# Performance work log

Hardware: AMD Instinct MI355X
Metric: run time of the kernel (lower is better)

Reference implementation:

```python
import jax, jax.numpy as jnp
import numpy as np

HEADS = 8
HEAD_DIM = 64
INNER = HEADS * HEAD_DIM  # 512
DIM = 512
B, H, W = 8, 32, 32
KV_LEN, KV_DIM = 77, 1024


def group_norm(x, g, b, groups=32, eps=1e-6):
    # x: [B, C, H, W]
    Bx, C, Hx, Wx = x.shape
    xr = x.reshape(Bx, groups, C // groups, Hx, Wx)
    mu = xr.mean(axis=(2, 3, 4), keepdims=True)
    var = xr.var(axis=(2, 3, 4), keepdims=True)
    xr = (xr - mu) * jax.lax.rsqrt(var + eps)
    return xr.reshape(Bx, C, Hx, Wx) * g[None, :, None, None] + b[None, :, None, None]


def layer_norm(x, g, b, eps=1e-5):
    mu = x.mean(axis=-1, keepdims=True)
    var = x.var(axis=-1, keepdims=True)
    return (x - mu) * jax.lax.rsqrt(var + eps) * g + b


def attention(qx, kvx, Wq, Wk, Wv, Wo, bo):
    # qx: [B, Sq, dim_q], kvx: [B, Sk, dim_kv]
    q = qx @ Wq
    k = kvx @ Wk
    v = kvx @ Wv
    Bx, Sq, _ = q.shape
    Sk = k.shape[1]
    q = q.reshape(Bx, Sq, HEADS, HEAD_DIM)
    k = k.reshape(Bx, Sk, HEADS, HEAD_DIM)
    v = v.reshape(Bx, Sk, HEADS, HEAD_DIM)
    att = jnp.einsum('bqhd,bkhd->bhqk', q, k) * (HEAD_DIM ** -0.5)
    att = jax.nn.softmax(att.astype(jnp.float32), axis=-1).astype(q.dtype)
    o = jnp.einsum('bhqk,bkhd->bqhd', att, v).reshape(Bx, Sq, INNER)
    return o @ Wo + bo


def setup_inputs() -> dict:
    key = jax.random.key(0)
    ks = jax.random.split(key, 20)
    s = 0.02
    def n(k, shape):
        return jax.random.normal(k, shape, jnp.float32) * s
    return {
        'q': jax.random.normal(ks[0], (B, DIM, H, W), jnp.float32),
        'kv': jax.random.normal(ks[1], (B, KV_LEN, KV_DIM), jnp.float32),
        'gn_g': jnp.ones((DIM,), jnp.float32), 'gn_b': jnp.zeros((DIM,), jnp.float32),
        'ln2_g': jnp.ones((INNER,), jnp.float32), 'ln2_b': jnp.zeros((INNER,), jnp.float32),
        'ln3_g': jnp.ones((INNER,), jnp.float32), 'ln3_b': jnp.zeros((INNER,), jnp.float32),
        'ln4_g': jnp.ones((INNER,), jnp.float32), 'ln4_b': jnp.zeros((INNER,), jnp.float32),
        'fc_in_w': n(ks[2], (DIM, INNER)), 'fc_in_b': jnp.zeros((INNER,), jnp.float32),
        'fc_out_w': n(ks[3], (INNER, DIM)), 'fc_out_b': jnp.zeros((DIM,), jnp.float32),
        'a1_q': n(ks[4], (INNER, INNER)), 'a1_k': n(ks[5], (INNER, INNER)),
        'a1_v': n(ks[6], (INNER, INNER)), 'a1_o': n(ks[7], (INNER, INNER)),
        'a1_ob': jnp.zeros((INNER,), jnp.float32),
        'a2_q': n(ks[8], (INNER, INNER)), 'a2_k': n(ks[9], (KV_DIM, INNER)),
        'a2_v': n(ks[10], (KV_DIM, INNER)), 'a2_o': n(ks[11], (INNER, INNER)),
        'a2_ob': jnp.zeros((INNER,), jnp.float32),
        'ff_proj_w': n(ks[12], (INNER, INNER * 8)), 'ff_proj_b': jnp.zeros((INNER * 8,), jnp.float32),
        'ff_out_w': n(ks[13], (INNER * 4, INNER)), 'ff_out_b': jnp.zeros((INNER,), jnp.float32),
    }


def reference(q, kv, gn_g, gn_b, ln2_g, ln2_b, ln3_g, ln3_b, ln4_g, ln4_b,
              fc_in_w, fc_in_b, fc_out_w, fc_out_b,
              a1_q, a1_k, a1_v, a1_o, a1_ob,
              a2_q, a2_k, a2_v, a2_o, a2_ob,
              ff_proj_w, ff_proj_b, ff_out_w, ff_out_b):
    res = q
    Bx, C, Hx, Wx = q.shape
    x = group_norm(q, gn_g, gn_b)
    x = x.reshape(Bx, C, Hx * Wx).transpose(0, 2, 1)  # [B, S, C]
    x = x @ fc_in_w + fc_in_b
    t = layer_norm(x, ln2_g, ln2_b)
    x = attention(t, t, a1_q, a1_k, a1_v, a1_o, a1_ob) + x
    x = attention(layer_norm(x, ln3_g, ln3_b), kv, a2_q, a2_k, a2_v, a2_o, a2_ob) + x
    h = layer_norm(x, ln4_g, ln4_b) @ ff_proj_w + ff_proj_b
    a, gate = jnp.split(h, 2, axis=-1)
    x = (a * jax.nn.gelu(gate, approximate=False)) @ ff_out_w + ff_out_b + x
    x = x @ fc_out_w + fc_out_b
    x = x.transpose(0, 2, 1).reshape(Bx, C, Hx, Wx)
    return x + res
```

## Files before the change

### kernel.cpp

```cpp
#include <hip/hip_runtime.h>
#include <cstdint>
#include <cstddef>

typedef __attribute__((ext_vector_type(8))) short bf16x8;
typedef __attribute__((ext_vector_type(4))) short short4v;
typedef __attribute__((ext_vector_type(4))) float f32x4;

__device__ __forceinline__ short f2b(float f) {
    unsigned u = __builtin_bit_cast(unsigned, f);
    u = (u + 0x7FFFu + ((u >> 16) & 1u)) >> 16;
    return (short)u;
}
__device__ __forceinline__ float b2f(short s) {
    unsigned u = ((unsigned)(unsigned short)s) << 16;
    return __builtin_bit_cast(float, u);
}

__device__ __forceinline__ void gload16(const short* g, short* l) {
    __builtin_amdgcn_global_load_lds(
        (const __attribute__((address_space(1))) unsigned int*)g,
        (__attribute__((address_space(3))) unsigned int*)l, 16, 0, 0);
}

__device__ __forceinline__ float gelu_fast(float g) {
    float g2 = g * g;
    float gp = g * (0.7978845608f + 0.0356774081f * g2);
    float e = exp2f(2.885390082f * gp);
    float th = 1.f - 2.f / (e + 1.f);
    return 0.5f * g * (1.f + th);
}

__device__ __forceinline__ int pn_ffp(int n) {
    int m = (n < 2048) ? n : (n - 2048);
    int gofs = (n < 2048) ? 0 : 32;
    int x = m >> 6, c = m & 63;
    return x * 128 + ((c >> 5) << 6) + gofs + (c & 31);
}

struct PrepArgs {
    const float* src[12];
    short* dst[12];
    const float* kv;
    short* kvb;
    const float* fb;
    float* bp;
};

__global__ __launch_bounds__(256) void prep(PrepArgs a) {
    int t = blockIdx.x;
    int tid = threadIdx.x;
    if (t >= 6144) {
        if (t >= 6452) {
            int n = (t - 6452) * 256 + tid;
            if (n < 4096) a.bp[pn_ffp(n)] = a.fb[n];
            return;
        }
        int idx = (t - 6144) * 256 + tid;
        if (idx >= 78848) return;
        const float4* s = (const float4*)a.kv + (size_t)idx * 2;
        float4 va = s[0], vb = s[1];
        bf16x8 w;
        w[0] = f2b(va.x); w[1] = f2b(va.y); w[2] = f2b(va.z); w[3] = f2b(va.w);
        w[4] = f2b(vb.x); w[5] = f2b(vb.y); w[6] = f2b(vb.z); w[7] = f2b(vb.w);
        *(bf16x8*)(a.kvb + (size_t)idx * 8) = w;
        return;
    }
    const int jstart[12] = {0, 256, 512, 768, 1024, 1280, 1536, 1792, 2304, 2816, 3072, 5120};
    const int jK[12] = {512, 512, 512, 512, 512, 512, 512, 1024, 1024, 512, 512, 2048};
    const int jN[12] = {512, 512, 512, 512, 512, 512, 512, 512, 512, 512, 4096, 512};
    int j = 11;
#pragma unroll
    for (int i = 11; i >= 1; --i)
        if (t < jstart[i]) j = i - 1;
    int tx = t - jstart[j];
    int K = jK[j], N = jN[j];
    int tn = N >> 5;
    int n0 = (tx % tn) * 32, k0 = (tx / tn) * 32;
    const float* w = a.src[j];
    short* wt = a.dst[j];
    bool perm = (j == 10);

    __shared__ float tile[32][33];
    int cx = tid & 31, ty0 = tid >> 5;
#pragma unroll
    for (int i = 0; i < 4; ++i) {
        int r = ty0 + i * 8;
        tile[r][cx] = w[(size_t)(k0 + r) * N + n0 + cx];
    }
    __syncthreads();
#pragma unroll
    for (int i = 0; i < 4; ++i) {
        int r = ty0 + i * 8;
        int drow = perm ? pn_ffp(n0 + r) : (n0 + r);
        wt[(size_t)drow * K + k0 + cx] = f2b(tile[cx][r]);
    }
}

__global__ __launch_bounds__(256) void gn_stats(const float* __restrict__ q,
                                                const float* __restrict__ g,
                                                const float* __restrict__ bta,
                                                float* __restrict__ sc,
                                                float* __restrict__ sh) {
    int bb = blockIdx.x >> 5, gg = blockIdx.x & 31;
    const float4* src = (const float4*)(q + ((size_t)(bb * 512 + gg * 16)) * 1024);
    float s = 0.f, s2 = 0.f;
#pragma unroll
    for (int i = 0; i < 16; ++i) {
        float4 v = src[threadIdx.x + 256 * i];
        s += (v.x + v.y) + (v.z + v.w);
        s2 += (v.x * v.x + v.y * v.y) + (v.z * v.z + v.w * v.w);
    }
#pragma unroll
    for (int m = 1; m < 64; m <<= 1) {
        s += __shfl_xor(s, m);
        s2 += __shfl_xor(s2, m);
    }
    __shared__ float red[8];
    int wv = threadIdx.x >> 6;
    if ((threadIdx.x & 63) == 0) { red[wv] = s; red[4 + wv] = s2; }
    __syncthreads();
    if (threadIdx.x < 16) {
        float S = red[0] + red[1] + red[2] + red[3];
        float S2 = red[4] + red[5] + red[6] + red[7];
        float mu = S * (1.f / 16384.f);
        float var = S2 * (1.f / 16384.f) - mu * mu;
        float rs = rsqrtf(var + 1e-6f);
        int c = gg * 16 + threadIdx.x;
        float scale = rs * g[c];
        sc[bb * 512 + c] = scale;
        sh[bb * 512 + c] = bta[c] - mu * scale;
    }
}

__global__ __launch_bounds__(256) void gn_apply(const float* __restrict__ q,
                                                const float* __restrict__ sc,
                                                const float* __restrict__ sh,
                                                short* __restrict__ out) {
    __shared__ short tile[512][33];
    int b = blockIdx.x >> 5, st = blockIdx.x & 31;
    int s0 = st * 32;
    int sl = threadIdx.x & 31, cg = threadIdx.x >> 5;
    for (int c = cg; c < 512; c += 8) {
        float v = q[((size_t)(b * 512 + c)) * 1024 + s0 + sl];
        float y = v * sc[b * 512 + c] + sh[b * 512 + c];
        tile[c][sl] = f2b(y);
    }
    __syncthreads();
    int sr = threadIdx.x >> 3, ch = threadIdx.x & 7;
    short* orow = out + ((size_t)(b * 1024 + s0 + sr)) * 512;
    for (int c8 = ch * 64; c8 < ch * 64 + 64; c8 += 8) {
        bf16x8 o;
#pragma unroll
        for (int jj = 0; jj < 8; ++jj) o[jj] = tile[c8 + jj][sr];
        *(bf16x8*)&orow[c8] = o;
    }
}

__global__ __launch_bounds__(256) void ln_rows(const float* __restrict__ x,
                                               const float* __restrict__ g,
                                               const float* __restrict__ bta,
                                               short* __restrict__ out) {
    int row = blockIdx.x * 4 + (threadIdx.x >> 6);
    int lane = threadIdx.x & 63;
    const float4* xr = (const float4*)(x + (size_t)row * 512);
    float4 v0 = xr[lane * 2], v1 = xr[lane * 2 + 1];
    float s = (v0.x + v0.y) + (v0.z + v0.w) + (v1.x + v1.y) + (v1.z + v1.w);
    float s2 = (v0.x * v0.x + v0.y * v0.y) + (v0.z * v0.z + v0.w * v0.w) +
               (v1.x * v1.x + v1.y * v1.y) + (v1.z * v1.z + v1.w * v1.w);
#pragma unroll
    for (int m = 1; m < 64; m <<= 1) {
        s += __shfl_xor(s, m);
        s2 += __shfl_xor(s2, m);
    }
    float mu = s * (1.f / 512.f);
    float var = s2 * (1.f / 512.f) - mu * mu;
    float rs = rsqrtf(var + 1e-5f);
    float4 ga = ((const float4*)g)[lane * 2], gb = ((const float4*)g)[lane * 2 + 1];
    float4 ba = ((const float4*)bta)[lane * 2], bb = ((const float4*)bta)[lane * 2 + 1];
    bf16x8 o;
    o[0] = f2b((v0.x - mu) * rs * ga.x + ba.x);
    o[1] = f2b((v0.y - mu) * rs * ga.y + ba.y);
    o[2] = f2b((v0.z - mu) * rs * ga.z + ba.z);
    o[3] = f2b((v0.w - mu) * rs * ga.w + ba.w);
    o[4] = f2b((v1.x - mu) * rs * gb.x + bb.x);
    o[5] = f2b((v1.y - mu) * rs * gb.y + bb.y);
    o[6] = f2b((v1.z - mu) * rs * gb.z + bb.z);
    o[7] = f2b((v1.w - mu) * rs * gb.w + bb.w);
    *(bf16x8*)(out + (size_t)row * 512 + lane * 8) = o;
}

template <int BN>
__global__ __launch_bounds__(256, 1) void gemm_gl(
    const short* __restrict__ A, const short* __restrict__ BT,
    int M, int N, int K,
    const float* __restrict__ bias,
    const float* __restrict__ addSrc,
    float* __restrict__ outF,
    short* __restrict__ outB,
    const float* __restrict__ resid,
    float* __restrict__ outFinal,
    int mode) {
    constexpr int FJ = BN / 32;
    constexpr int ASZ = 3 * 128 * 32;
    constexpr int BSZ = 3 * BN * 32;
    __shared__ __attribute__((aligned(16))) short smem[ASZ + BSZ];
    short* Asb = smem;
    short* Bsb = smem + ASZ;
    int tid = threadIdx.x;
    int wave = tid >> 6, lane = tid & 63;
    int wr = wave >> 1, wc = wave & 1;
    int m0 = blockIdx.y * 128, n0 = blockIdx.x * BN;
    f32x4 acc[4][FJ];
#pragma unroll
    for (int i = 0; i < 4; ++i)
#pragma unroll
        for (int j = 0; j < FJ; ++j) acc[i][j] = (f32x4){0.f, 0.f, 0.f, 0.f};

    int srow = tid >> 2;
    int scg = (((tid & 3) ^ ((tid >> 3) & 3)) << 3);
    int ar0 = m0 + srow; if (ar0 >= M) ar0 = M - 1;
    int ar1 = m0 + 64 + srow; if (ar1 >= M) ar1 = M - 1;
    const short* ag0 = A + (size_t)ar0 * K + scg;
    const short* ag1 = A + (size_t)ar1 * K + scg;
    const short* bg0 = BT + (size_t)(n0 + srow) * K + scg;
    const short* bg1 = BT + (size_t)(n0 + 64 + srow) * K + scg;
    int nk = K >> 5;

    auto stage = [&](int buf) {
        gload16(ag0, &Asb[buf * 4096 + wave * 512]);
        gload16(ag1, &Asb[buf * 4096 + 2048 + wave * 512]);
        gload16(bg0, &Bsb[buf * (BN * 32) + wave * 512]);
        if constexpr (BN == 128) gload16(bg1, &Bsb[buf * 4096 + 2048 + wave * 512]);
        ag0 += 32; ag1 += 32; bg0 += 32; bg1 += 32;
    };
    stage(0);
    stage(1);

    int lr = lane & 15, g = lane >> 4;
    int cur = 0;
    for (int kt = 0; kt < nk; ++kt) {
        __builtin_amdgcn_sched_barrier(0);
        if (kt + 1 < nk) {
            if constexpr (BN == 128) asm volatile("s_waitcnt vmcnt(4)" ::: "memory");
            else asm volatile("s_waitcnt vmcnt(3)" ::: "memory");
        } else {
            asm volatile("s_waitcnt vmcnt(0)" ::: "memory");
        }
        __builtin_amdgcn_sched_barrier(0);
        __builtin_amdgcn_s_barrier();
        int n2 = cur + 2; if (n2 >= 3) n2 -= 3;
        if (kt + 2 < nk) stage(n2);
        bf16x8 af[4], bfr[FJ];
#pragma unroll
        for (int i = 0; i < 4; ++i) {
            int row = wr * 64 + i * 16 + lr;
            af[i] = *(const bf16x8*)&Asb[cur * 4096 + row * 32 + ((g ^ ((row >> 1) & 3)) << 3)];
        }
#pragma unroll
        for (int j = 0; j < FJ; ++j) {
            int row = wc * (BN / 2) + j * 16 + lr;
            bfr[j] = *(const bf16x8*)&Bsb[cur * (BN * 32) + row * 32 + ((g ^ ((row >> 1) & 3)) << 3)];
        }
#pragma unroll
        for (int i = 0; i < 4; ++i)
#pragma unroll
            for (int j = 0; j < FJ; ++j)
                acc[i][j] = __builtin_amdgcn_mfma_f32_16x16x32_bf16(af[i], bfr[j], acc[i][j], 0, 0, 0);
        cur = cur + 1; if (cur >= 3) cur -= 3;
    }

    int lq = lane >> 4;
    if (mode == 1) {
#pragma unroll
        for (int i = 0; i < 4; ++i)
#pragma unroll
            for (int j = 0; j < FJ; ++j) {
                int mm0 = m0 + wr * 64 + i * 16 + lq * 4;
                int nn = n0 + wc * (BN / 2) + j * 16 + lr;
                int bb = mm0 >> 10, ss = mm0 & 1023;
                size_t oi = ((size_t)(bb * 512 + nn)) * 1024 + ss;
                float bv = bias ? bias[nn] : 0.f;
                float4 rv = *(const float4*)&resid[oi];
                float4 ov;
                ov.x = acc[i][j][0] + bv + rv.x;
                ov.y = acc[i][j][1] + bv + rv.y;
                ov.z = acc[i][j][2] + bv + rv.z;
                ov.w = acc[i][j][3] + bv + rv.w;
                *(float4*)&outFinal[oi] = ov;
            }
        return;
    }
    if (mode == 2) {
        if constexpr (FJ == 4) {
            short* eb = smem;
            __syncthreads();
#pragma unroll
            for (int i = 0; i < 4; ++i)
#pragma unroll
                for (int j = 0; j < 2; ++j)
#pragma unroll
                    for (int r = 0; r < 4; ++r) {
                        int slot = wc * 64 + j * 16 + lr;
                        float a = acc[i][j][r] + bias[n0 + slot];
                        float gt = acc[i][j + 2][r] + bias[n0 + slot + 32];
                        float ge = gelu_fast(gt);
                        eb[(wr * 64 + i * 16 + lq * 4 + r) * 72 + wc * 32 + j * 16 + lr] =
                            f2b(a * ge);
                    }
            __syncthreads();
#pragma unroll
            for (int q = 0; q < 4; ++q) {
                int idx = q * 256 + tid;
                int row = idx >> 3, cq = (idx & 7) * 8;
                bf16x8 o = *(bf16x8*)&eb[row * 72 + cq];
                *(bf16x8*)&outB[(size_t)(m0 + row) * 2048 + blockIdx.x * 64 + cq] = o;
            }
        }
        return;
    }
    {
        constexpr int EC = BN + 4;
        float* ef = (float*)smem;
#pragma unroll
        for (int h = 0; h < 2; ++h) {
            __syncthreads();
            if (wr == h) {
#pragma unroll
                for (int i = 0; i < 4; ++i)
#pragma unroll
                    for (int j = 0; j < FJ; ++j)
#pragma unroll
                        for (int r = 0; r < 4; ++r)
                            ef[(i * 16 + lq * 4 + r) * EC + wc * (BN / 2) + j * 16 + lr] =
                                acc[i][j][r];
            }
            __syncthreads();
#pragma unroll
            for (int q = 0; q < BN / 16; ++q) {
                int idx = q * 256 + tid;
                int row = idx / (BN / 4);
                int cq = (idx % (BN / 4)) * 4;
                int mm = m0 + h * 64 + row;
                if (mm >= M) continue;
                int nn = n0 + cq;
                float4 v = *(float4*)&ef[row * EC + cq];
                if (bias) {
                    float4 b4 = *(const float4*)&bias[nn];
                    v.x += b4.x; v.y += b4.y; v.z += b4.z; v.w += b4.w;
                }
                size_t ig = (size_t)mm * N + nn;
                if (addSrc) {
                    float4 a4 = *(const float4*)&addSrc[ig];
                    v.x += a4.x; v.y += a4.y; v.z += a4.z; v.w += a4.w;
                }
                if (outF) *(float4*)&outF[ig] = v;
                if (outB) {
                    short4v o = {f2b(v.x), f2b(v.y), f2b(v.z), f2b(v.w)};
                    *(short4v*)&outB[ig] = o;
                }
            }
        }
    }
}

__global__ __launch_bounds__(256, 1) void attn_mfma(const short* __restrict__ qp,
                                                    const short* __restrict__ kp,
                                                    const short* __restrict__ vp,
                                                    short* __restrict__ op,
                                                    int kv_len, int kvBatchRows,
                                                    int qStride, int kvStride) {
    __shared__ __attribute__((aligned(16))) short Kt[64][72];
    __shared__ __attribute__((aligned(16))) short Vt[64][72];
    __shared__ __attribute__((aligned(16))) short Pt[4][2][16][72];
    int tid = threadIdx.x, w = tid >> 6, lane = tid & 63;
    int g = lane >> 4, c = lane & 15;
    int bh = blockIdx.y, b = bh >> 3, h = bh & 7;
    int q0 = blockIdx.x * 128 + w * 16;

    const float QS = 0.125f * 1.44269504f;
    bf16x8 qa[2][2];
#pragma unroll
    for (int qi = 0; qi < 2; ++qi) {
        const short* qbase = qp + ((size_t)(b * 1024 + q0 + qi * 64 + c)) * qStride + h * 64;
        bf16x8 qr0 = *(const bf16x8*)(qbase + g * 8);
        bf16x8 qr1 = *(const bf16x8*)(qbase + 32 + g * 8);
#pragma unroll
        for (int j = 0; j < 8; ++j) {
            qa[qi][0][j] = f2b(b2f(qr0[j]) * QS);
            qa[qi][1][j] = f2b(b2f(qr1[j]) * QS);
        }
    }

    f32x4 oac[2][4];
#pragma unroll
    for (int qi = 0; qi < 2; ++qi)
#pragma unroll
        for (int dt = 0; dt < 4; ++dt) oac[qi][dt] = (f32x4){0.f, 0.f, 0.f, 0.f};
    float l[2][4];
#pragma unroll
    for (int qi = 0; qi < 2; ++qi)
#pragma unroll
        for (int r = 0; r < 4; ++r) l[qi][r] = 0.f;

    int skey = tid & 63, sd0 = (tid >> 6) * 16;
    int ntile = (kv_len + 63) >> 6;
    size_t kvbase = (size_t)b * kvBatchRows;

    bf16x8 k0, k1, v0, v1;
    {
        int krow = skey < kv_len ? skey : kv_len - 1;
        const short* kpp = kp + (kvbase + krow) * kvStride + h * 64 + sd0;
        const short* vpp = vp + (kvbase + krow) * kvStride + h * 64 + sd0;
        k0 = *(const bf16x8*)kpp; k1 = *(const bf16x8*)(kpp + 8);
        v0 = *(const bf16x8*)vpp; v1 = *(const bf16x8*)(vpp + 8);
    }

    for (int kt = 0; kt < ntile; ++kt) {
        __syncthreads();
        *(bf16x8*)&Kt[skey][sd0] = k0;
        *(bf16x8*)&Kt[skey][sd0 + 8] = k1;
#pragma unroll
        for (int j = 0; j < 8; ++j) {
            Vt[sd0 + j][skey] = v0[j];
            Vt[sd0 + 8 + j][skey] = v1[j];
        }
        __syncthreads();
        if (kt + 1 < ntile) {
            int krow = (kt + 1) * 64 + skey;
            if (krow >= kv_len) krow = kv_len - 1;
            const short* kpp = kp + (kvbase + krow) * kvStride + h * 64 + sd0;
            const short* vpp = vp + (kvbase + krow) * kvStride + h * 64 + sd0;
            k0 = *(const bf16x8*)kpp; k1 = *(const bf16x8*)(kpp + 8);
            v0 = *(const bf16x8*)vpp; v1 = *(const bf16x8*)(vpp + 8);
        }

        f32x4 s[2][4];
#pragma unroll
        for (int nt = 0; nt < 4; ++nt) {
            bf16x8 kb0 = *(const bf16x8*)&Kt[nt * 16 + c][g * 8];
            bf16x8 kb1 = *(const bf16x8*)&Kt[nt * 16 + c][32 + g * 8];
#pragma unroll
            for (int qi = 0; qi < 2; ++qi) {
                s[qi][nt] = __builtin_amdgcn_mfma_f32_16x16x32_bf16(
                    qa[qi][0], kb0, (f32x4){0.f, 0.f, 0.f, 0.f}, 0, 0, 0);
                s[qi][nt] = __builtin_amdgcn_mfma_f32_16x16x32_bf16(
                    qa[qi][1], kb1, s[qi][nt], 0, 0, 0);
            }
        }
        if (kt * 64 + 64 > kv_len) {
#pragma unroll
            for (int nt = 0; nt < 4; ++nt) {
                bool valid = kt * 64 + nt * 16 + c < kv_len;
#pragma unroll
                for (int qi = 0; qi < 2; ++qi)
#pragma unroll
                    for (int r = 0; r < 4; ++r) {
                        float pv = valid ? exp2f(s[qi][nt][r]) : 0.f;
                        s[qi][nt][r] = pv;
                        l[qi][r] += pv;
                    }
            }
        } else {
#pragma unroll
            for (int nt = 0; nt < 4; ++nt)
#pragma unroll
                for (int qi = 0; qi < 2; ++qi)
#pragma unroll
                    for (int r = 0; r < 4; ++r) {
                        float pv = exp2f(s[qi][nt][r]);
                        s[qi][nt][r] = pv;
                        l[qi][r] += pv;
                    }
        }

        bf16x8 pa[2][2];
#pragma unroll
        for (int qi = 0; qi < 2; ++qi) {
#pragma unroll
            for (int nt = 0; nt < 4; ++nt)
#pragma unroll
                for (int r = 0; r < 4; ++r)
                    Pt[w][qi][4 * g + r][nt * 16 + c] = f2b(s[qi][nt][r]);
        }
#pragma unroll
        for (int qi = 0; qi < 2; ++qi) {
            pa[qi][0] = *(const bf16x8*)&Pt[w][qi][c][g * 8];
            pa[qi][1] = *(const bf16x8*)&Pt[w][qi][c][32 + g * 8];
        }
#pragma unroll
        for (int dt = 0; dt < 4; ++dt) {
            bf16x8 vb0 = *(const bf16x8*)&Vt[dt * 16 + c][g * 8];
            bf16x8 vb1 = *(const bf16x8*)&Vt[dt * 16 + c][32 + g * 8];
#pragma unroll
            for (int qi = 0; qi < 2; ++qi) {
                oac[qi][dt] = __builtin_amdgcn_mfma_f32_16x16x32_bf16(pa[qi][0], vb0, oac[qi][dt], 0, 0, 0);
                oac[qi][dt] = __builtin_amdgcn_mfma_f32_16x16x32_bf16(pa[qi][1], vb1, oac[qi][dt], 0, 0, 0);
            }
        }
    }

#pragma unroll
    for (int mk = 1; mk < 16; mk <<= 1)
#pragma unroll
        for (int qi = 0; qi < 2; ++qi)
#pragma unroll
            for (int r = 0; r < 4; ++r) l[qi][r] += __shfl_xor(l[qi][r], mk);
#pragma unroll
    for (int qi = 0; qi < 2; ++qi)
#pragma unroll
        for (int r = 0; r < 4; ++r) {
            float inv = 1.f / l[qi][r];
            short* orow = op + ((size_t)(b * 1024 + q0 + qi * 64 + 4 * g + r)) * 512 + h * 64;
#pragma unroll
            for (int dt = 0; dt < 4; ++dt)
                orow[dt * 16 + c] = f2b(oac[qi][dt][r] * inv);
        }
}

extern "C" void kernel_launch(void* const* d_in, const int* in_sizes, int n_in,
                              void* d_out, int out_size, void* d_ws, size_t ws_size,
                              hipStream_t stream) {
    (void)in_sizes; (void)n_in; (void)out_size; (void)ws_size;
    const float* q_in = (const float*)d_in[0];
    const float* kv_in = (const float*)d_in[1];
    const float* gn_g = (const float*)d_in[2];
    const float* gn_b = (const float*)d_in[3];
    const float* ln2_g = (const float*)d_in[4];
    const float* ln2_b = (const float*)d_in[5];
    const float* ln3_g = (const float*)d_in[6];
    const float* ln3_b = (const float*)d_in[7];
    const float* ln4_g = (const float*)d_in[8];
    const float* ln4_b = (const float*)d_in[9];
    const float* fc_in_w = (const float*)d_in[10];
    const float* fc_in_b = (const float*)d_in[11];
    const float* fc_out_w = (const float*)d_in[12];
    const float* fc_out_b = (const float*)d_in[13];
    const float* a1_qw = (const float*)d_in[14];
    const float* a1_kw = (const float*)d_in[15];
    const float* a1_vw = (const float*)d_in[16];
    const float* a1_ow = (const float*)d_in[17];
    const float* a1_ob = (const float*)d_in[18];
    const float* a2_qw = (const float*)d_in[19];
    const float* a2_kw = (const float*)d_in[20];
    const float* a2_vw = (const float*)d_in[21];
    const float* a2_ow = (const float*)d_in[22];
    const float* a2_ob = (const float*)d_in[23];
    const float* ffp_w = (const float*)d_in[24];
    const float* ffp_b = (const float*)d_in[25];
    const float* ffo_w = (const float*)d_in[26];
    const float* ffo_b = (const float*)d_in[27];
    float* out = (float*)d_out;

    char* p = (char*)d_ws;
    auto alloc = [&](size_t n) {
        char* r = p;
        p += (n + 255) & ~(size_t)255;
        return r;
    };
    short* wt_fci = (short*)alloc((size_t)512 * 512 * 2);
    short* wt_fco = (short*)alloc((size_t)512 * 512 * 2);
    short* wt_qkv = (short*)alloc((size_t)1536 * 512 * 2);
    short* wt_a1o = (short*)alloc((size_t)512 * 512 * 2);
    short* wt_a2q = (short*)alloc((size_t)512 * 512 * 2);
    short* wt_kv2 = (short*)alloc((size_t)1024 * 1024 * 2);
    short* wt_a2o = (short*)alloc((size_t)512 * 512 * 2);
    short* wt_ffp = (short*)alloc((size_t)4096 * 512 * 2);
    short* wt_ffo = (short*)alloc((size_t)512 * 2048 * 2);
    float* biasP = (float*)alloc((size_t)4096 * 4);
    float* x = (float*)alloc((size_t)8192 * 512 * 4);
    short* tb = (short*)alloc((size_t)8192 * 512 * 2);
    short* qkvbuf = (short*)alloc((size_t)8192 * 1536 * 2);
    short* qbuf = (short*)alloc((size_t)8192 * 512 * 2);
    short* kvpbuf = (short*)alloc((size_t)616 * 1024 * 2);
    short* obuf = (short*)alloc((size_t)8192 * 512 * 2);
    short* kvb = (short*)alloc((size_t)616 * 1024 * 2);
    short* ggb = (short*)alloc((size_t)8192 * 2048 * 2);
    float* gnsc = (float*)alloc((size_t)8 * 512 * 4);
    float* gnsh = (float*)alloc((size_t)8 * 512 * 4);

    PrepArgs pa;
    pa.src[0] = fc_in_w;  pa.dst[0] = wt_fci;
    pa.src[1] = fc_out_w; pa.dst[1] = wt_fco;
    pa.src[2] = a1_qw;    pa.dst[2] = wt_qkv;
    pa.src[3] = a1_kw;    pa.dst[3] = wt_qkv + (size_t)512 * 512;
    pa.src[4] = a1_vw;    pa.dst[4] = wt_qkv + (size_t)1024 * 512;
    pa.src[5] = a1_ow;    pa.dst[5] = wt_a1o;
    pa.src[6] = a2_qw;    pa.dst[6] = wt_a2q;
    pa.src[7] = a2_kw;    pa.dst[7] = wt_kv2;
    pa.src[8] = a2_vw;    pa.dst[8] = wt_kv2 + (size_t)512 * 1024;
    pa.src[9] = a2_ow;    pa.dst[9] = wt_a2o;
    pa.src[10] = ffp_w;   pa.dst[10] = wt_ffp;
    pa.src[11] = ffo_w;   pa.dst[11] = wt_ffo;
    pa.kv = kv_in; pa.kvb = kvb; pa.fb = ffp_b; pa.bp = biasP;
    prep<<<6468, 256, 0, stream>>>(pa);

    auto gemm128n = [&](const short* A, const short* BT, int M, int N, int K,
                        const float* bias, const float* addSrc, float* outF, short* outB,
                        const float* resid, float* outFinal, int mode) {
        dim3 g(N / 128, (M + 127) / 128);
        gemm_gl<128><<<g, 256, 0, stream>>>(A, BT, M, N, K, bias, addSrc, outF, outB,
                                            resid, outFinal, mode);
    };
    auto gemm64n = [&](const short* A, const short* BT, int M, int N, int K,
                       const float* bias, const float* addSrc, float* outF, short* outB,
                       const float* resid, float* outFinal, int mode) {
        dim3 g(N / 64, (M + 127) / 128);
        gemm_gl<64><<<g, 256, 0, stream>>>(A, BT, M, N, K, bias, addSrc, outF, outB,
                                           resid, outFinal, mode);
    };

    gn_stats<<<256, 256, 0, stream>>>(q_in, gn_g, gn_b, gnsc, gnsh);
    gn_apply<<<256, 256, 0, stream>>>(q_in, gnsc, gnsh, tb);
    gemm64n(tb, wt_fci, 8192, 512, 512, fc_in_b, nullptr, x, nullptr, nullptr, nullptr, 0);
    ln_rows<<<2048, 256, 0, stream>>>(x, ln2_g, ln2_b, tb);
    gemm128n(tb, wt_qkv, 8192, 1536, 512, nullptr, nullptr, nullptr, qkvbuf, nullptr, nullptr, 0);
    attn_mfma<<<dim3(8, 64), 256, 0, stream>>>(qkvbuf, qkvbuf + 512, qkvbuf + 1024, obuf,
                                               1024, 1024, 1536, 1536);
    gemm64n(obuf, wt_a1o, 8192, 512, 512, a1_ob, x, x, nullptr, nullptr, nullptr, 0);
    ln_rows<<<2048, 256, 0, stream>>>(x, ln3_g, ln3_b, tb);
    gemm64n(tb, wt_a2q, 8192, 512, 512, nullptr, nullptr, nullptr, qbuf, nullptr, nullptr, 0);
    gemm128n(kvb, wt_kv2, 616, 1024, 1024, nullptr, nullptr, nullptr, kvpbuf, nullptr, nullptr, 0);
    attn_mfma<<<dim3(8, 64), 256, 0, stream>>>(qbuf, kvpbuf, kvpbuf + 512, obuf,
                                               77, 77, 512, 1024);
    gemm64n(obuf, wt_a2o, 8192, 512, 512, a2_ob, x, x, nullptr, nullptr, nullptr, 0);
    ln_rows<<<2048, 256, 0, stream>>>(x, ln4_g, ln4_b, tb);
    gemm128n(tb, wt_ffp, 8192, 4096, 512, biasP, nullptr, nullptr, ggb, nullptr, nullptr, 2);
    gemm128n(ggb, wt_ffo, 8192, 512, 2048, ffo_b, x, nullptr, tb, nullptr, nullptr, 0);
    gemm64n(tb, wt_fco, 8192, 512, 512, fc_out_b, nullptr, nullptr, nullptr, q_in, out, 1);
}
```

Before: 316.6 us.

## Store residual stream in bf16, add 128x256 GEMM kernel, vectorize weight prep

The residual stream x moves from fp32 to bf16, which halves the memory traffic of the layer-norm reads and the residual add/store in the GEMM epilogues. A new 512-thread GEMM kernel with 128x256 tiles handles the QKV projection and the FF projection with its fused GEGLU epilogue. The weight-transpose prep kernel now writes four bf16 values per store. Keeping the residual in bf16 adds rounding error at every residual add, which may affect accuracy.

```diff
diff --git a/kernel.cpp b/kernel.cpp
--- a/kernel.cpp
+++ b/kernel.cpp
@@ -88,12 +88,12 @@
         tile[r][cx] = w[(size_t)(k0 + r) * N + n0 + cx];
     }
     __syncthreads();
-#pragma unroll
-    for (int i = 0; i < 4; ++i) {
-        int r = ty0 + i * 8;
-        int drow = perm ? pn_ffp(n0 + r) : (n0 + r);
-        wt[(size_t)drow * K + k0 + cx] = f2b(tile[cx][r]);
-    }
+    int r = tid >> 3;
+    int kg = (tid & 7) * 4;
+    int drow = perm ? pn_ffp(n0 + r) : (n0 + r);
+    short4v o = {f2b(tile[kg][r]), f2b(tile[kg + 1][r]),
+                 f2b(tile[kg + 2][r]), f2b(tile[kg + 3][r])};
+    *(short4v*)&wt[(size_t)drow * K + k0 + kg] = o;
 }
 
 __global__ __launch_bounds__(256) void gn_stats(const float* __restrict__ q,
@@ -156,17 +156,19 @@
     }
 }
 
-__global__ __launch_bounds__(256) void ln_rows(const float* __restrict__ x,
+__global__ __launch_bounds__(256) void ln_rows(const short* __restrict__ x,
                                                const float* __restrict__ g,
                                                const float* __restrict__ bta,
                                                short* __restrict__ out) {
     int row = blockIdx.x * 4 + (threadIdx.x >> 6);
     int lane = threadIdx.x & 63;
-    const float4* xr = (const float4*)(x + (size_t)row * 512);
-    float4 v0 = xr[lane * 2], v1 = xr[lane * 2 + 1];
-    float s = (v0.x + v0.y) + (v0.z + v0.w) + (v1.x + v1.y) + (v1.z + v1.w);
-    float s2 = (v0.x * v0.x + v0.y * v0.y) + (v0.z * v0.z + v0.w * v0.w) +
-               (v1.x * v1.x + v1.y * v1.y) + (v1.z * v1.z + v1.w * v1.w);
+    bf16x8 v8 = *(const bf16x8*)(x + (size_t)row * 512 + lane * 8);
+    float v[8];
+#pragma unroll
+    for (int j = 0; j < 8; ++j) v[j] = b2f(v8[j]);
+    float s = 0.f, s2 = 0.f;
+#pragma unroll
+    for (int j = 0; j < 8; ++j) { s += v[j]; s2 += v[j] * v[j]; }
 #pragma unroll
     for (int m = 1; m < 64; m <<= 1) {
         s += __shfl_xor(s, m);
@@ -178,14 +180,14 @@
     float4 ga = ((const float4*)g)[lane * 2], gb = ((const float4*)g)[lane * 2 + 1];
     float4 ba = ((const float4*)bta)[lane * 2], bb = ((const float4*)bta)[lane * 2 + 1];
     bf16x8 o;
-    o[0] = f2b((v0.x - mu) * rs * ga.x + ba.x);
-    o[1] = f2b((v0.y - mu) * rs * ga.y + ba.y);
-    o[2] = f2b((v0.z - mu) * rs * ga.z + ba.z);
-    o[3] = f2b((v0.w - mu) * rs * ga.w + ba.w);
-    o[4] = f2b((v1.x - mu) * rs * gb.x + bb.x);
-    o[5] = f2b((v1.y - mu) * rs * gb.y + bb.y);
-    o[6] = f2b((v1.z - mu) * rs * gb.z + bb.z);
-    o[7] = f2b((v1.w - mu) * rs * gb.w + bb.w);
+    o[0] = f2b((v[0] - mu) * rs * ga.x + ba.x);
+    o[1] = f2b((v[1] - mu) * rs * ga.y + ba.y);
+    o[2] = f2b((v[2] - mu) * rs * ga.z + ba.z);
+    o[3] = f2b((v[3] - mu) * rs * ga.w + ba.w);
+    o[4] = f2b((v[4] - mu) * rs * gb.x + bb.x);
+    o[5] = f2b((v[5] - mu) * rs * gb.y + bb.y);
+    o[6] = f2b((v[6] - mu) * rs * gb.z + bb.z);
+    o[7] = f2b((v[7] - mu) * rs * gb.w + bb.w);
     *(bf16x8*)(out + (size_t)row * 512 + lane * 8) = o;
 }
 
@@ -194,8 +196,7 @@
     const short* __restrict__ A, const short* __restrict__ BT,
     int M, int N, int K,
     const float* __restrict__ bias,
-    const float* __restrict__ addSrc,
-    float* __restrict__ outF,
+    const short* __restrict__ addSrcB,
     short* __restrict__ outB,
     const float* __restrict__ resid,
     float* __restrict__ outFinal,
@@ -290,34 +291,6 @@
             }
         return;
     }
-    if (mode == 2) {
-        if constexpr (FJ == 4) {
-            short* eb = smem;
-            __syncthreads();
-#pragma unroll
-            for (int i = 0; i < 4; ++i)
-#pragma unroll
-                for (int j = 0; j < 2; ++j)
-#pragma unroll
-                    for (int r = 0; r < 4; ++r) {
-                        int slot = wc * 64 + j * 16 + lr;
-                        float a = acc[i][j][r] + bias[n0 + slot];
-                        float gt = acc[i][j + 2][r] + bias[n0 + slot + 32];
-                        float ge = gelu_fast(gt);
-                        eb[(wr * 64 + i * 16 + lq * 4 + r) * 72 + wc * 32 + j * 16 + lr] =
-                            f2b(a * ge);
-                    }
-            __syncthreads();
-#pragma unroll
-            for (int q = 0; q < 4; ++q) {
-                int idx = q * 256 + tid;
-                int row = idx >> 3, cq = (idx & 7) * 8;
-                bf16x8 o = *(bf16x8*)&eb[row * 72 + cq];
-                *(bf16x8*)&outB[(size_t)(m0 + row) * 2048 + blockIdx.x * 64 + cq] = o;
-            }
-        }
-        return;
-    }
     {
         constexpr int EC = BN + 4;
         float* ef = (float*)smem;
@@ -349,15 +322,154 @@
                     v.x += b4.x; v.y += b4.y; v.z += b4.z; v.w += b4.w;
                 }
                 size_t ig = (size_t)mm * N + nn;
-                if (addSrc) {
-                    float4 a4 = *(const float4*)&addSrc[ig];
-                    v.x += a4.x; v.y += a4.y; v.z += a4.z; v.w += a4.w;
+                if (addSrcB) {
+                    short4v a4 = *(const short4v*)&addSrcB[ig];
+                    v.x += b2f(a4[0]); v.y += b2f(a4[1]);
+                    v.z += b2f(a4[2]); v.w += b2f(a4[3]);
                 }
-                if (outF) *(float4*)&outF[ig] = v;
-                if (outB) {
-                    short4v o = {f2b(v.x), f2b(v.y), f2b(v.z), f2b(v.w)};
-                    *(short4v*)&outB[ig] = o;
+                short4v o = {f2b(v.x), f2b(v.y), f2b(v.z), f2b(v.w)};
+                *(short4v*)&outB[ig] = o;
+            }
+        }
+    }
+}
+
+__global__ __launch_bounds__(512, 1) void gemm256w(
+    const short* __restrict__ A, const short* __restrict__ BT,
+    int M, int N, int K,
+    const float* __restrict__ bias,
+    short* __restrict__ outB,
+    int mode) {
+    __shared__ __attribute__((aligned(16))) short smem[3 * 4096 + 3 * 8192];
+    short* Asb = smem;
+    short* Bsb = smem + 12288;
+    int tid = threadIdx.x;
+    int wave = tid >> 6, lane = tid & 63;
+    int wrM = wave >> 2, wcN = wave & 3;
+    int m0 = blockIdx.y * 128, n0 = blockIdx.x * 256;
+    f32x4 acc[4][4];
+#pragma unroll
+    for (int i = 0; i < 4; ++i)
+#pragma unroll
+        for (int j = 0; j < 4; ++j) acc[i][j] = (f32x4){0.f, 0.f, 0.f, 0.f};
+
+    const short* gp[3];
+    int ldsoff[3];
+    bool isA[3];
+#pragma unroll
+    for (int s = 0; s < 3; ++s) {
+        int qq = wave * 3 + s;
+        bool a = qq < 8;
+        int r = (a ? qq : qq - 8) * 16 + (lane >> 2);
+        int sc = (((lane & 3) ^ ((r >> 1) & 3)) << 3);
+        gp[s] = a ? (A + (size_t)(m0 + r) * K + sc)
+                  : (BT + (size_t)(n0 + r) * K + sc);
+        ldsoff[s] = (a ? qq : (qq - 8)) * 512;
+        isA[s] = a;
+    }
+    int nk = K >> 5;
+    auto stage = [&](int buf) {
+#pragma unroll
+        for (int s = 0; s < 3; ++s) {
+            short* l = isA[s] ? &Asb[buf * 4096 + ldsoff[s]]
+                              : &Bsb[buf * 8192 + ldsoff[s]];
+            gload16(gp[s], l);
+            gp[s] += 32;
+        }
+    };
+    stage(0);
+    stage(1);
+
+    int lr = lane & 15, g = lane >> 4;
+    int cur = 0;
+    for (int kt = 0; kt < nk; ++kt) {
+        __builtin_amdgcn_sched_barrier(0);
+        if (kt + 1 < nk) {
+            asm volatile("s_waitcnt vmcnt(3)" ::: "memory");
+        } else {
+            asm volatile("s_waitcnt vmcnt(0)" ::: "memory");
+        }
+        __builtin_amdgcn_sched_barrier(0);
+        __builtin_amdgcn_s_barrier();
+        int n2 = cur + 2; if (n2 >= 3) n2 -= 3;
+        if (kt + 2 < nk) stage(n2);
+        bf16x8 af[4], bfr[4];
+#pragma unroll
+        for (int i = 0; i < 4; ++i) {
+            int row = wrM * 64 + i * 16 + lr;
+            af[i] = *(const bf16x8*)&Asb[cur * 4096 + row * 32 + ((g ^ ((row >> 1) & 3)) << 3)];
+        }
+#pragma unroll
+        for (int j = 0; j < 4; ++j) {
+            int row = wcN * 64 + j * 16 + lr;
+            bfr[j] = *(const bf16x8*)&Bsb[cur * 8192 + row * 32 + ((g ^ ((row >> 1) & 3)) << 3)];
+        }
+#pragma unroll
+        for (int i = 0; i < 4; ++i)
+#pragma unroll
+            for (int j = 0; j < 4; ++j)
+                acc[i][j] = __builtin_amdgcn_mfma_f32_16x16x32_bf16(af[i], bfr[j], acc[i][j], 0, 0, 0);
+        cur = cur + 1; if (cur >= 3) cur -= 3;
+    }
+
+    int lq = lane >> 4;
+    if (mode == 2) {
+        short* eb = smem;
+        int xhalf = wcN >> 1, half = wcN & 1;
+        __syncthreads();
+#pragma unroll
+        for (int i = 0; i < 4; ++i)
+#pragma unroll
+            for (int j = 0; j < 2; ++j)
+#pragma unroll
+                for (int r = 0; r < 4; ++r) {
+                    int slot = n0 + wcN * 64 + j * 16 + lr;
+                    float a = acc[i][j][r] + bias[slot];
+                    float gt = acc[i][j + 2][r] + bias[slot + 32];
+                    float ge = gelu_fast(gt);
+                    int row = wrM * 64 + i * 16 + lq * 4 + r;
+                    int col = xhalf * 64 + half * 32 + j * 16 + lr;
+                    eb[row * 136 + col] = f2b(a * ge);
                 }
+        __syncthreads();
+#pragma unroll
+        for (int q = 0; q < 4; ++q) {
+            int idx = q * 512 + tid;
+            int row = idx >> 4, cg = (idx & 15) * 8;
+            bf16x8 o = *(bf16x8*)&eb[row * 136 + cg];
+            *(bf16x8*)&outB[(size_t)(m0 + row) * 2048 + blockIdx.x * 128 + cg] = o;
+        }
+        return;
+    }
+    {
+        float* ef = (float*)smem;
+#pragma unroll
+        for (int h = 0; h < 2; ++h) {
+            __syncthreads();
+            if (wrM == h) {
+#pragma unroll
+                for (int i = 0; i < 4; ++i)
+#pragma unroll
+                    for (int j = 0; j < 4; ++j)
+#pragma unroll
+                        for (int r = 0; r < 4; ++r)
+                            ef[(i * 16 + lq * 4 + r) * 260 + wcN * 64 + j * 16 + lr] =
+                                acc[i][j][r];
+            }
+            __syncthreads();
+#pragma unroll
+            for (int q = 0; q < 8; ++q) {
+                int idx = q * 512 + tid;
+                int row = idx >> 6;
+                int cq = (idx & 63) * 4;
+                float4 v = *(float4*)&ef[row * 260 + cq];
+                int nn = n0 + cq;
+                if (bias) {
+                    float4 b4 = *(const float4*)&bias[nn];
+                    v.x += b4.x; v.y += b4.y; v.z += b4.z; v.w += b4.w;
+                }
+                short4v o = {f2b(v.x), f2b(v.y), f2b(v.z), f2b(v.w)};
+                *(short4v*)&outB[(size_t)(m0 + h * 64 + row) * N + nn] = o;
             }
         }
     }
@@ -567,7 +679,7 @@
     short* wt_ffp = (short*)alloc((size_t)4096 * 512 * 2);
     short* wt_ffo = (short*)alloc((size_t)512 * 2048 * 2);
     float* biasP = (float*)alloc((size_t)4096 * 4);
-    float* x = (float*)alloc((size_t)8192 * 512 * 4);
+    short* xb = (short*)alloc((size_t)8192 * 512 * 2);
     short* tb = (short*)alloc((size_t)8192 * 512 * 2);
     short* qkvbuf = (short*)alloc((size_t)8192 * 1536 * 2);
     short* qbuf = (short*)alloc((size_t)8192 * 512 * 2);
@@ -595,36 +707,38 @@
     prep<<<6468, 256, 0, stream>>>(pa);
 
     auto gemm128n = [&](const short* A, const short* BT, int M, int N, int K,
-                        const float* bias, const float* addSrc, float* outF, short* outB,
+                        const float* bias, const short* addSrcB, short* outB,
                         const float* resid, float* outFinal, int mode) {
         dim3 g(N / 128, (M + 127) / 128);
-        gemm_gl<128><<<g, 256, 0, stream>>>(A, BT, M, N, K, bias, addSrc, outF, outB,
+        gemm_gl<128><<<g, 256, 0, stream>>>(A, BT, M, N, K, bias, addSrcB, outB,
                                             resid, outFinal, mode);
     };
     auto gemm64n = [&](const short* A, const short* BT, int M, int N, int K,
-                       const float* bias, const float* addSrc, float* outF, short* outB,
+                       const float* bias, const short* addSrcB, short* outB,
                        const float* resid, float* outFinal, int mode) {
         dim3 g(N / 64, (M + 127) / 128);
-        gemm_gl<64><<<g, 256, 0, stream>>>(A, BT, M, N, K, bias, addSrc, outF, outB,
+        gemm_gl<64><<<g, 256, 0, stream>>>(A, BT, M, N, K, bias, addSrcB, outB,
                                            resid, outFinal, mode);
     };
 
     gn_stats<<<256, 256, 0, stream>>>(q_in, gn_g, gn_b, gnsc, gnsh);
     gn_apply<<<256, 256, 0, stream>>>(q_in, gnsc, gnsh, tb);
-    gemm64n(tb, wt_fci, 8192, 512, 512, fc_in_b, nullptr, x, nullptr, nullptr, nullptr, 0);
-    ln_rows<<<2048, 256, 0, stream>>>(x, ln2_g, ln2_b, tb);
-    gemm128n(tb, wt_qkv, 8192, 1536, 512, nullptr, nullptr, nullptr, qkvbuf, nullptr, nullptr, 0);
+    gemm64n(tb, wt_fci, 8192, 512, 512, fc_in_b, nullptr, xb, nullptr, nullptr, 0);
+    ln_rows<<<2048, 256, 0, stream>>>(xb, ln2_g, ln2_b, tb);
+    gemm256w<<<dim3(6, 64), 512, 0, stream>>>(tb, wt_qkv, 8192, 1536, 512,
+                                              nullptr, qkvbuf, 0);
     attn_mfma<<<dim3(8, 64), 256, 0, stream>>>(qkvbuf, qkvbuf + 512, qkvbuf + 1024, obuf,
                                                1024, 1024, 1536, 1536);
-    gemm64n(obuf, wt_a1o, 8192, 512, 512, a1_ob, x, x, nullptr, nullptr, nullptr, 0);
-    ln_rows<<<2048, 256, 0, stream>>>(x, ln3_g, ln3_b, tb);
-    gemm64n(tb, wt_a2q, 8192, 512, 512, nullptr, nullptr, nullptr, qbuf, nullptr, nullptr, 0);
-    gemm128n(kvb, wt_kv2, 616, 1024, 1024, nullptr, nullptr, nullptr, kvpbuf, nullptr, nullptr, 0);
+    gemm64n(obuf, wt_a1o, 8192, 512, 512, a1_ob, xb, xb, nullptr, nullptr, 0);
+    ln_rows<<<2048, 256, 0, stream>>>(xb, ln3_g, ln3_b, tb);
+    gemm64n(tb, wt_a2q, 8192, 512, 512, nullptr, nullptr, qbuf, nullptr, nullptr, 0);
+    gemm128n(kvb, wt_kv2, 616, 1024, 1024, nullptr, nullptr, kvpbuf, nullptr, nullptr, 0);
     attn_mfma<<<dim3(8, 64), 256, 0, stream>>>(qbuf, kvpbuf, kvpbuf + 512, obuf,
                                                77, 77, 512, 1024);
-    gemm64n(obuf, wt_a2o, 8192, 512, 512, a2_ob, x, x, nullptr, nullptr, nullptr, 0);
-    ln_rows<<<2048, 256, 0, stream>>>(x, ln4_g, ln4_b, tb);
-    gemm128n(tb, wt_ffp, 8192, 4096, 512, biasP, nullptr, nullptr, ggb, nullptr, nullptr, 2);
-    gemm128n(ggb, wt_ffo, 8192, 512, 2048, ffo_b, x, nullptr, tb, nullptr, nullptr, 0);
-    gemm64n(tb, wt_fco, 8192, 512, 512, fc_out_b, nullptr, nullptr, nullptr, q_in, out, 1);
-}
+    gemm64n(obuf, wt_a2o, 8192, 512, 512, a2_ob, xb, xb, nullptr, nullptr, 0);
+    ln_rows<<<2048, 256, 0, stream>>>(xb, ln4_g, ln4_b, tb);
+    gemm256w<<<dim3(16, 64), 512, 0, stream>>>(tb, wt_ffp, 8192, 4096, 512,
+                                               biasP, ggb, 2);
+    gemm128n(ggb, wt_ffo, 8192, 512, 2048, ffo_b, xb, tb, nullptr, nullptr, 0);
+    gemm64n(tb, wt_fco, 8192, 512, 512, fc_out_b, nullptr, nullptr, q_in, out, 1);
+}
```

After: 305.9 us. 1.04x faster.
